# Kernel optimization log

Hardware: AMD Instinct MI355X
Metric: run time of the kernel (lower is better)

Reference implementation:

```python
import jax, jax.numpy as jnp
import numpy as np

B, S, E, HEADS = 2, 2048, 2048, 16


def setup_inputs() -> dict:
    key = jax.random.key(0)
    k1, k2, k3 = jax.random.split(key, 3)
    x = jax.random.normal(k1, (B, S, E), dtype=jnp.float32)
    # Linear weights stored as (in, out); torch uses y = x @ W.T with W (out, in) -- same math.
    W_qkvh = jax.random.normal(k2, (E, 3 * E + HEADS), dtype=jnp.float32) * (E ** -0.5)
    W_out = jax.random.normal(k3, (E, E), dtype=jnp.float32) * (E ** -0.5)
    return {"x": x, "W_qkvh": W_qkvh, "W_out": W_out}


def reference(x, W_qkvh, W_out):
    b, s, e = x.shape
    heads = W_qkvh.shape[1] - 3 * e
    d = e // heads
    scale = e ** 0.5

    proj = x @ W_qkvh                                  # (b, s, 3e + heads)
    QKV, Hg = proj[..., : 3 * e], proj[..., 3 * e:]
    Hg = jnp.tanh(Hg).transpose(0, 2, 1)[..., None]    # (b, h, s, 1) gate
    QKV = QKV.reshape(b, s, heads, 3 * d).transpose(0, 2, 1, 3)  # (b, h, s, 3d)
    Q, K, V = jnp.split(QKV, 3, axis=-1)               # each (b, h, s, d)

    # Cummean(H*K) along seq: cumsum(n * x) / n^2 with n = 1..s
    n = jnp.arange(1, s + 1, dtype=x.dtype).reshape(1, 1, s, 1)
    Kc = jnp.cumsum(n * (Hg * K), axis=2) / (n * n)    # (b, h, s, d)

    scores = jnp.einsum('bhqd,bhkd->bhqk', Q, Kc) / scale
    causal = jnp.triu(jnp.ones((s, s), dtype=bool), k=1)
    scores = jnp.where(causal, -jnp.inf, scores)
    attn = jax.nn.softmax(scores, axis=-1)

    out = jnp.einsum('bhqk,bhkd->bhqd', attn, V)       # (b, h, s, d)
    out = out.transpose(0, 2, 1, 3).reshape(b, s, e)
    return out @ W_out
```

## Files before the change

kernel.cpp:

```cpp
#include <hip/hip_runtime.h>
#include <hip/hip_bf16.h>
#include <math.h>

#define PB 2
#define PS 2048
#define PE 2048
#define PH 16
#define PD 128
#define PN_PROJ 6160
#define PM 4096

typedef __attribute__((ext_vector_type(8))) short bf16x8;
typedef __attribute__((ext_vector_type(4))) float f32x4;

__device__ __forceinline__ void gload_lds16(const void* g, void* l) {
  __builtin_amdgcn_global_load_lds((const __attribute__((address_space(1))) void*)g,
                                   (__attribute__((address_space(3))) void*)l, 16, 0, 0);
}

__global__ __launch_bounds__(512, 1) void gemm_qkv(
    const __hip_bfloat16* __restrict__ A, const __hip_bfloat16* __restrict__ Bt,
    __hip_bfloat16* __restrict__ Qp, __hip_bfloat16* __restrict__ Kp,
    __hip_bfloat16* __restrict__ Vtp, int K, int nTilesX) {
  constexpr int BM = 128, BN = 384, WM = 2, WN = 4;
  constexpr int MF = BM / WM / 16;
  constexpr int NF = BN / WN / 16;
  constexpr int SLOT = (BM + BN) * 64;
  constexpr int AL = BM / 64;
  constexpr int BL = BN / 64;
  constexpr int NLD = AL + BL;

  __shared__ __align__(16) __hip_bfloat16 lds[2 * SLOT];

  const int tid = threadIdx.x;
  const int w = tid >> 6, lane = tid & 63;
  const int fq = lane >> 4, fr = lane & 15;
  const int wm = w / WN, wn = w % WN;

  const int xcd = blockIdx.x & 7;
  const int local = blockIdx.x >> 3;
  const int h = xcd * 2 + (local >> 5);
  const int mBase = (local & 31) * BM;
  const int nBase = h * BN;

  const int srow = tid >> 3, sc = tid & 7;

  auto stage = [&](int t) {
    char* base = (char*)lds + (size_t)(t & 1) * SLOT * 2;
#pragma unroll
    for (int l = 0; l < AL; ++l) {
      int row = l * 64 + srow;
      int cs = sc ^ (row & 7);
      gload_lds16(A + (size_t)(mBase + row) * K + t * 64 + cs * 8,
                  base + l * 8192 + w * 1024);
    }
#pragma unroll
    for (int l = 0; l < BL; ++l) {
      int row = l * 64 + srow;
      int cs = sc ^ (row & 7);
      gload_lds16(Bt + (size_t)(nBase + row) * K + t * 64 + cs * 8,
                  base + BM * 128 + l * 8192 + w * 1024);
    }
  };

  f32x4 acc[MF][NF];
#pragma unroll
  for (int m = 0; m < MF; ++m)
#pragma unroll
    for (int n = 0; n < NF; ++n) acc[m][n] = (f32x4){0.f, 0.f, 0.f, 0.f};

  const int NT = K / 64;
  stage(0); stage(1);

#pragma unroll 1
  for (int t = 0; t < NT; ++t) {
    if (t + 1 < NT) asm volatile("s_waitcnt vmcnt(%0)" ::"i"(NLD) : "memory");
    else            asm volatile("s_waitcnt vmcnt(0)" ::: "memory");
    __builtin_amdgcn_s_barrier();
    __builtin_amdgcn_sched_barrier(0);

    const __hip_bfloat16* sl = lds + (size_t)(t & 1) * SLOT;

    bf16x8 av[MF], bv[NF];
#pragma unroll
    for (int m = 0; m < MF; ++m) {
      int row = wm * (BM / WM) + m * 16 + fr;
      av[m] = *(const bf16x8*)&sl[row * 64 + ((fq ^ (row & 7)) * 8)];
    }
#pragma unroll
    for (int n = 0; n < NF; ++n) {
      int row = wn * (BN / WN) + n * 16 + fr;
      bv[n] = *(const bf16x8*)&sl[BM * 64 + row * 64 + ((fq ^ (row & 7)) * 8)];
    }
    asm volatile("s_waitcnt lgkmcnt(0)" ::: "memory");
    __builtin_amdgcn_sched_barrier(0);
    __builtin_amdgcn_s_setprio(1);
#pragma unroll
    for (int m = 0; m < MF; ++m)
#pragma unroll
      for (int n = 0; n < NF; ++n)
        acc[m][n] = __builtin_amdgcn_mfma_f32_16x16x32_bf16(av[m], bv[n], acc[m][n], 0, 0, 0);
    __builtin_amdgcn_s_setprio(0);

#pragma unroll
    for (int m = 0; m < MF; ++m) {
      int row = wm * (BM / WM) + m * 16 + fr;
      av[m] = *(const bf16x8*)&sl[row * 64 + (((4 + fq) ^ (row & 7)) * 8)];
    }
#pragma unroll
    for (int n = 0; n < NF; ++n) {
      int row = wn * (BN / WN) + n * 16 + fr;
      bv[n] = *(const bf16x8*)&sl[BM * 64 + row * 64 + (((4 + fq) ^ (row & 7)) * 8)];
    }
    asm volatile("s_waitcnt lgkmcnt(0)" ::: "memory");
    __builtin_amdgcn_s_barrier();
    __builtin_amdgcn_sched_barrier(0);
    if (t + 2 < NT) stage(t + 2);
    __builtin_amdgcn_s_setprio(1);
#pragma unroll
    for (int m = 0; m < MF; ++m)
#pragma unroll
      for (int n = 0; n < NF; ++n)
        acc[m][n] = __builtin_amdgcn_mfma_f32_16x16x32_bf16(av[m], bv[n], acc[m][n], 0, 0, 0);
    __builtin_amdgcn_s_setprio(0);
  }

#pragma unroll
  for (int m = 0; m < MF; ++m) {
#pragma unroll
    for (int n = 0; n < NF; ++n) {
      int row0 = mBase + wm * (BM / WM) + m * 16 + fq * 4;
      int colL = wn * (BN / WN) + n * 16 + fr;
      int which = colL >> 7;
      int d = colL & 127;
      int b = row0 >> 11, s0 = row0 & (PS - 1);
      if (which == 2) {
        union { __hip_bfloat16 hh[4]; uint2 u; } pk;
#pragma unroll
        for (int j = 0; j < 4; ++j) pk.hh[j] = __float2bfloat16(acc[m][n][j]);
        *(uint2*)&Vtp[(((size_t)(b * PH + h)) * PD + d) * PS + s0] = pk.u;
      } else {
        __hip_bfloat16* dst = which == 0 ? Qp : Kp;
#pragma unroll
        for (int j = 0; j < 4; ++j)
          dst[(((size_t)(b * PH + h)) * PS + s0 + j) * PD + d] = __float2bfloat16(acc[m][n][j]);
      }
    }
  }
}

template <int BM, int BN, int WM, int WN, typename OutT>
__global__ __launch_bounds__(512, 1) void gemm_cs3(
    const __hip_bfloat16* __restrict__ A, const __hip_bfloat16* __restrict__ Bt,
    OutT* __restrict__ C, int K, int lda, int ldb, int ldc, int nTilesX) {
  constexpr int MF = BM / WM / 16;
  constexpr int NF = BN / WN / 16;
  constexpr int SLOT = (BM + BN) * 64;
  constexpr int AL = BM / 64;
  constexpr int BL = BN / 64;
  constexpr int NLD = AL + BL;

  __shared__ __align__(16) __hip_bfloat16 lds[3 * SLOT];

  const int tid = threadIdx.x;
  const int w = tid >> 6, lane = tid & 63;
  const int fq = lane >> 4, fr = lane & 15;
  const int wm = w / WN, wn = w % WN;

  const int xcd = blockIdx.x & 7;
  const int local = blockIdx.x >> 3;
  const int nPerX = nTilesX >> 3;
  const int nTY = (gridDim.x >> 3) / nPerX;
  const int mBase = (local % nTY) * BM;
  const int nBase = (xcd * nPerX + local / nTY) * BN;

  const int srow = tid >> 3, sc = tid & 7;

  auto stage = [&](int t) {
    char* base = (char*)lds + (size_t)(t % 3) * SLOT * 2;
#pragma unroll
    for (int l = 0; l < AL; ++l) {
      int row = l * 64 + srow;
      int cs = sc ^ (row & 7);
      gload_lds16(A + (size_t)(mBase + row) * lda + t * 64 + cs * 8,
                  base + l * 8192 + w * 1024);
    }
#pragma unroll
    for (int l = 0; l < BL; ++l) {
      int row = l * 64 + srow;
      int cs = sc ^ (row & 7);
      gload_lds16(Bt + (size_t)(nBase + row) * ldb + t * 64 + cs * 8,
                  base + BM * 128 + l * 8192 + w * 1024);
    }
  };

  f32x4 acc[MF][NF];
#pragma unroll
  for (int m = 0; m < MF; ++m)
#pragma unroll
    for (int n = 0; n < NF; ++n) acc[m][n] = (f32x4){0.f, 0.f, 0.f, 0.f};

  const int NT = K / 64;
  stage(0); stage(1);

#pragma unroll 1
  for (int t = 0; t < NT; ++t) {
    if (t + 1 < NT) asm volatile("s_waitcnt vmcnt(%0)" ::"i"(NLD) : "memory");
    else            asm volatile("s_waitcnt vmcnt(0)" ::: "memory");
    __builtin_amdgcn_s_barrier();
    __builtin_amdgcn_sched_barrier(0);
    if (t + 2 < NT) stage(t + 2);

    const __hip_bfloat16* sl = lds + (size_t)(t % 3) * SLOT;

#pragma unroll
    for (int kk = 0; kk < 2; ++kk) {
      bf16x8 av[MF], bv[NF];
#pragma unroll
      for (int m = 0; m < MF; ++m) {
        int row = wm * (BM / WM) + m * 16 + fr;
        av[m] = *(const bf16x8*)&sl[row * 64 + (((kk * 4 + fq) ^ (row & 7)) * 8)];
      }
#pragma unroll
      for (int n = 0; n < NF; ++n) {
        int row = wn * (BN / WN) + n * 16 + fr;
        bv[n] = *(const bf16x8*)&sl[BM * 64 + row * 64 + (((kk * 4 + fq) ^ (row & 7)) * 8)];
      }
      asm volatile("s_waitcnt lgkmcnt(0)" ::: "memory");
      __builtin_amdgcn_sched_barrier(0);
      __builtin_amdgcn_s_setprio(1);
#pragma unroll
      for (int m = 0; m < MF; ++m)
#pragma unroll
        for (int n = 0; n < NF; ++n)
          acc[m][n] = __builtin_amdgcn_mfma_f32_16x16x32_bf16(av[m], bv[n], acc[m][n], 0, 0, 0);
      __builtin_amdgcn_s_setprio(0);
    }
  }

#pragma unroll
  for (int m = 0; m < MF; ++m) {
#pragma unroll
    for (int n = 0; n < NF; ++n) {
      int row0 = mBase + wm * (BM / WM) + m * 16 + fq * 4;
      int col = nBase + wn * (BN / WN) + n * 16 + fr;
#pragma unroll
      for (int j = 0; j < 4; ++j) {
        if constexpr (__is_same(OutT, float))
          C[(size_t)(row0 + j) * ldc + col] = acc[m][n][j];
        else
          C[(size_t)(row0 + j) * ldc + col] = __float2bfloat16(acc[m][n][j]);
      }
    }
  }
}

__global__ __launch_bounds__(256) void transpose_cast(const float* __restrict__ W,
                                                      __hip_bfloat16* __restrict__ Wt,
                                                      int ldw, int ldt, int nOff) {
  __shared__ float t[32][33];
  int nb = blockIdx.x * 32, kb = blockIdx.y * 32;
  int tx = threadIdx.x & 31, ty = threadIdx.x >> 5;
#pragma unroll
  for (int i = 0; i < 4; ++i) {
    int k = ty + i * 8;
    t[k][tx] = W[(size_t)(kb + k) * ldw + nOff + nb + tx];
  }
  __syncthreads();
#pragma unroll
  for (int i = 0; i < 4; ++i) {
    int n = ty + i * 8;
    Wt[(size_t)(nb + n) * ldt + kb + tx] = __float2bfloat16(t[tx][n]);
  }
}

__global__ __launch_bounds__(256) void hg_from_x(const float* __restrict__ x,
                                                 const float* __restrict__ W,
                                                 float* __restrict__ hgbuf,
                                                 __hip_bfloat16* __restrict__ xb) {
  int bs = blockIdx.x;
  int b = bs >> 11, s = bs & (PS - 1);
  __shared__ float xs[PE];
  __shared__ float red[16][17];
  const float* xr = x + (size_t)bs * PE;
  for (int i = threadIdx.x; i < PE / 4; i += 256)
    *(float4*)&xs[i * 4] = ((const float4*)xr)[i];
  __syncthreads();
  {
    union { __hip_bfloat16 hh[8]; bf16x8 v; } pk;
#pragma unroll
    for (int k = 0; k < 8; ++k) pk.hh[k] = __float2bfloat16(xs[threadIdx.x * 8 + k]);
    *(bf16x8*)&xb[(size_t)bs * PE + threadIdx.x * 8] = pk.v;
  }
  int h = threadIdx.x & 15, part = threadIdx.x >> 4;
  float acc = 0.f;
  for (int k = part * 128; k < part * 128 + 128; ++k)
    acc += xs[k] * W[(size_t)k * PN_PROJ + 3 * PE + h];
  red[part][h] = acc;
  __syncthreads();
  if (threadIdx.x < 16) {
    float sm = 0.f;
#pragma unroll
    for (int p = 0; p < 16; ++p) sm += red[p][threadIdx.x];
    hgbuf[(size_t)(b * PH + threadIdx.x) * PS + s] = tanhf(sm);
  }
}

#define KC_SCALE 0.031879358f

__global__ __launch_bounds__(128) void kc_pass1(const __hip_bfloat16* __restrict__ Kp,
                                                const float* __restrict__ hgbuf,
                                                float* __restrict__ csum) {
  int c = blockIdx.x & 15, bh = blockIdx.x >> 4;
  int d = threadIdx.x;
  __shared__ float hgs[128];
  hgs[d] = hgbuf[(size_t)bh * PS + c * 128 + d];
  __syncthreads();
  const __hip_bfloat16* kb = Kp + ((size_t)bh * PS + c * 128) * PD + d;
  float acc = 0.f;
  int j0 = c * 128;
  for (int i = 0; i < 128; ++i)
    acc += (float)(j0 + i + 1) * hgs[i] * __bfloat162float(kb[(size_t)i * PD]);
  csum[blockIdx.x * 128 + d] = acc;
}

__global__ __launch_bounds__(128) void kc_pass2(__hip_bfloat16* __restrict__ Kp,
                                                const float* __restrict__ hgbuf,
                                                const float* __restrict__ csum) {
  int c = blockIdx.x & 15, bh = blockIdx.x >> 4;
  int d = threadIdx.x;
  __shared__ float hgs[128];
  hgs[d] = hgbuf[(size_t)bh * PS + c * 128 + d];
  __syncthreads();
  float acc = 0.f;
  for (int cc = 0; cc < c; ++cc) acc += csum[(bh * 16 + cc) * 128 + d];
  __hip_bfloat16* kb = Kp + ((size_t)bh * PS + c * 128) * PD + d;
  int j0 = c * 128;
  for (int i = 0; i < 128; ++i) {
    float t = (float)(j0 + i + 1);
    acc += t * hgs[i] * __bfloat162float(kb[(size_t)i * PD]);
    kb[(size_t)i * PD] = __float2bfloat16(acc / (t * t) * KC_SCALE);
  }
}

__global__ __launch_bounds__(512, 1) void attn_mfma(const __hip_bfloat16* __restrict__ Qp,
                                                    const __hip_bfloat16* __restrict__ Kp,
                                                    const __hip_bfloat16* __restrict__ Vtp,
                                                    __hip_bfloat16* __restrict__ O) {
  const int qt = 15 - (blockIdx.x >> 5);
  const int bh = blockIdx.x & 31;
  const int b = bh >> 4, h = bh & 15;
  const int tid = threadIdx.x;
  const int w = tid >> 6, lane = tid & 63;
  const int fq = lane >> 4, fr = lane & 15;
  const int nt = (qt + 1) * 2;
  const int q0 = qt * 128;
  const int qw = q0 + w * 16;

  __shared__ __align__(16) char smem[67584];
  __hip_bfloat16* Psw = (__hip_bfloat16*)(smem + 49152) + w * 16 * 72;
  __hip_bfloat16* Os = (__hip_bfloat16*)(smem + 16384);

  const __hip_bfloat16* kb0 = Kp + (size_t)bh * PS * PD;
  const __hip_bfloat16* vb0 = Vtp + (size_t)bh * PD * PS;

  auto stageK = [&](int t, int bufi) {
    char* ksb = smem + bufi * 16384;
    const __hip_bfloat16* kb = kb0 + (size_t)(t * 64) * PD;
#pragma unroll
    for (int p = 0; p < 2; ++p) {
      int s = p * 512 + tid;
      int row = s >> 4, c = s & 15;
      int cs = c ^ (row & 7);
      gload_lds16(kb + (size_t)row * PD + cs * 8,
                  ksb + (size_t)(p * 512 + (tid & ~63)) * 16);
    }
  };
  auto stageV = [&](int t) {
    char* vsb = smem + 32768;
    const __hip_bfloat16* vb = vb0 + t * 64;
#pragma unroll
    for (int p = 0; p < 2; ++p) {
      int s = p * 512 + tid;
      int row = s >> 3, c = s & 7;
      int cs = c ^ (row & 7);
      gload_lds16(vb + (size_t)row * PS + cs * 8,
                  vsb + (size_t)(p * 512 + (tid & ~63)) * 16);
    }
  };

  const __hip_bfloat16* qbase = Qp + ((size_t)bh * PS + qw) * PD;
  bf16x8 qf[4];
#pragma unroll
  for (int kk = 0; kk < 4; ++kk)
    qf[kk] = *(const bf16x8*)&qbase[(size_t)fr * PD + kk * 32 + fq * 8];

  stageK(0, 0);
  stageV(0);
  int cur = 0;

  f32x4 oacc[8];
#pragma unroll
  for (int nd = 0; nd < 8; ++nd) oacc[nd] = (f32x4){0.f, 0.f, 0.f, 0.f};
  float m_ = -__builtin_inff(), l_ = 0.f;

#pragma unroll 1
  for (int kt = 0; kt < nt; ++kt) {
    const bool hasNextK = (kt + 1 < nt);
    if (hasNextK) stageK(kt + 1, cur ^ 1);
    if (hasNextK) asm volatile("s_waitcnt vmcnt(4)" ::: "memory");
    else          asm volatile("s_waitcnt vmcnt(2)" ::: "memory");
    __builtin_amdgcn_s_barrier();
    __builtin_amdgcn_sched_barrier(0);

    const bool compute = (kt * 64 <= qw + 15);
    const bool diag = (kt * 64 + 63) > qw;
    const __hip_bfloat16* Ks = (const __hip_bfloat16*)(smem + cur * 16384);

    f32x4 sacc[4];
    if (compute) {
#pragma unroll
      for (int n = 0; n < 4; ++n) sacc[n] = (f32x4){0.f, 0.f, 0.f, 0.f};
#pragma unroll
      for (int kk = 0; kk < 4; ++kk) {
#pragma unroll
        for (int n = 0; n < 4; ++n) {
          bf16x8 kf = *(const bf16x8*)&Ks[(n * 16 + fr) * 128 + (((kk * 4 + fq) ^ (fr & 7)) * 8)];
          sacc[n] = __builtin_amdgcn_mfma_f32_16x16x32_bf16(kf, qf[kk], sacc[n], 0, 0, 0);
        }
      }
    }

    if (hasNextK) asm volatile("s_waitcnt vmcnt(2)" ::: "memory");
    else          asm volatile("s_waitcnt vmcnt(0)" ::: "memory");
    __builtin_amdgcn_s_barrier();
    __builtin_amdgcn_sched_barrier(0);

    if (compute) {
      const __hip_bfloat16* Vts = (const __hip_bfloat16*)(smem + 32768);
      const int qg = qw + fr;
      float sv[4][4];
#pragma unroll
      for (int n = 0; n < 4; ++n)
#pragma unroll
        for (int j = 0; j < 4; ++j) sv[n][j] = sacc[n][j];
      if (diag) {
#pragma unroll
        for (int n = 0; n < 4; ++n)
#pragma unroll
          for (int j = 0; j < 4; ++j)
            if ((kt * 64 + n * 16 + fq * 4 + j) > qg) sv[n][j] = -__builtin_inff();
      }
      float pmax = sv[0][0];
#pragma unroll
      for (int n = 0; n < 4; ++n)
#pragma unroll
        for (int j = 0; j < 4; ++j) pmax = fmaxf(pmax, sv[n][j]);
      pmax = fmaxf(pmax, __shfl_xor(pmax, 16, 64));
      pmax = fmaxf(pmax, __shfl_xor(pmax, 32, 64));

      const bool nof = __all(pmax <= m_ + 11.5415605f);
      const float mn = nof ? m_ : fmaxf(m_, pmax);
      float ps = 0.f;
#pragma unroll
      for (int n = 0; n < 4; ++n) {
        union { __hip_bfloat16 hh[4]; uint2 u; } pkk;
#pragma unroll
        for (int j = 0; j < 4; ++j) {
          float p = exp2f(sv[n][j] - mn);
          ps += p;
          pkk.hh[j] = __float2bfloat16(p);
        }
        *(uint2*)&Psw[fr * 72 + n * 16 + fq * 4] = pkk.u;
      }
      ps += __shfl_xor(ps, 16, 64);
      ps += __shfl_xor(ps, 32, 64);

      if (!nof) {
        const float alpha = exp2f(m_ - mn);
        l_ = l_ * alpha + ps;
        m_ = mn;
        float a0 = __shfl(alpha, fq * 4 + 0, 64);
        float a1 = __shfl(alpha, fq * 4 + 1, 64);
        float a2 = __shfl(alpha, fq * 4 + 2, 64);
        float a3 = __shfl(alpha, fq * 4 + 3, 64);
#pragma unroll
        for (int nd = 0; nd < 8; ++nd) {
          oacc[nd][0] *= a0; oacc[nd][1] *= a1;
          oacc[nd][2] *= a2; oacc[nd][3] *= a3;
        }
      } else {
        l_ += ps;
      }

#pragma unroll
      for (int kk2 = 0; kk2 < 2; ++kk2) {
        bf16x8 pa = *(const bf16x8*)&Psw[fr * 72 + kk2 * 32 + fq * 8];
#pragma unroll
        for (int nd = 0; nd < 8; ++nd) {
          bf16x8 vf = *(const bf16x8*)&Vts[(nd * 16 + fr) * 64 + (((kk2 * 4 + fq) ^ (fr & 7)) * 8)];
          oacc[nd] = __builtin_amdgcn_mfma_f32_16x16x32_bf16(pa, vf, oacc[nd], 0, 0, 0);
        }
      }
    }

    asm volatile("s_waitcnt lgkmcnt(0)" ::: "memory");
    __builtin_amdgcn_sched_barrier(0);
    __builtin_amdgcn_s_barrier();
    if (kt + 1 < nt) stageV(kt + 1);
    cur ^= 1;
  }

  float inv = 1.0f / l_;
  float inv4[4];
#pragma unroll
  for (int j = 0; j < 4; ++j) inv4[j] = __shfl(inv, fq * 4 + j, 64);
#pragma unroll
  for (int nd = 0; nd < 8; ++nd)
#pragma unroll
    for (int j = 0; j < 4; ++j)
      Os[(w * 16 + fq * 4 + j) * 136 + nd * 16 + fr] =
          __float2bfloat16(oacc[nd][j] * inv4[j]);
  __syncthreads();
#pragma unroll
  for (int it = 0; it < 4; ++it) {
    int i = it * 512 + tid;
    int row = i >> 4, ch = i & 15;
    *(bf16x8*)&O[(size_t)(b * PS + q0 + row) * PE + h * 128 + ch * 8] =
        *(const bf16x8*)&Os[row * 136 + ch * 8];
  }
}

extern "C" void kernel_launch(void* const* d_in, const int* in_sizes, int n_in,
                              void* d_out, int out_size, void* d_ws, size_t ws_size,
                              hipStream_t stream) {
  const float* x     = (const float*)d_in[0];
  const float* Wqkvh = (const float*)d_in[1];
  const float* Wout  = (const float*)d_in[2];
  float* out = (float*)d_out;

  const size_t HD = (size_t)PB * PH * PS * PD;
  char* wsb = (char*)d_ws;
  __hip_bfloat16* Qp = (__hip_bfloat16*)wsb;   wsb += HD * 2;
  __hip_bfloat16* Kp = (__hip_bfloat16*)wsb;   wsb += HD * 2;
  __hip_bfloat16* Vtp = (__hip_bfloat16*)wsb;  wsb += HD * 2;
  __hip_bfloat16* xb = (__hip_bfloat16*)wsb;   wsb += (size_t)PM * PE * 2;
  __hip_bfloat16* Wq_t = (__hip_bfloat16*)wsb; wsb += (size_t)3 * PE * PE * 2;
  __hip_bfloat16* Wout_t = (__hip_bfloat16*)wsb; wsb += (size_t)PE * PE * 2;
  float* hgbuf = (float*)wsb;                  wsb += (size_t)PB * PH * PS * 4;
  float* csum = (float*)wsb;

  hg_from_x<<<PM, 256, 0, stream>>>(x, Wqkvh, hgbuf, xb);
  transpose_cast<<<dim3(3 * PE / 32, PE / 32), 256, 0, stream>>>(Wqkvh, Wq_t, PN_PROJ, PE, 0);
  transpose_cast<<<dim3(PE / 32, PE / 32), 256, 0, stream>>>(Wout, Wout_t, PE, PE, 0);

  gemm_qkv<<<dim3((PM / 128) * PH), 512, 0, stream>>>(xb, Wq_t, Qp, Kp, Vtp, PE, PH);

  kc_pass1<<<PB * PH * 16, 128, 0, stream>>>(Kp, hgbuf, csum);
  kc_pass2<<<PB * PH * 16, 128, 0, stream>>>(Kp, hgbuf, csum);

  __hip_bfloat16* Ob = xb;
  attn_mfma<<<512, 512, 0, stream>>>(Qp, Kp, Vtp, Ob);

  gemm_cs3<128, 256, 2, 4, float>
      <<<dim3((PM / 128) * (PE / 256)), 512, 0, stream>>>(
          Ob, Wout_t, out, PE, PE, PE, PE, PE / 256);
}
```

Before: 294.7 us.

## Pair complementary causal query tiles per attention block for load balance

Each attention block now processes two query tiles, pk and 15-pk, sharing the K/V tiles staged into LDS across the longer tile's key range, and the grid is halved to 256 blocks. This evens out per-block work under the causal mask and reuses each staged K/V tile for two query groups. In exchange it doubles the accumulator and Q-fragment registers per thread, which risks spills under 512-thread launch bounds, and leaves fewer blocks to spread over the CUs.

```diff
diff --git a/kernel.cpp b/kernel.cpp
--- a/kernel.cpp
+++ b/kernel.cpp
@@ -347,15 +347,17 @@
                                                     const __hip_bfloat16* __restrict__ Kp,
                                                     const __hip_bfloat16* __restrict__ Vtp,
                                                     __hip_bfloat16* __restrict__ O) {
-  const int qt = 15 - (blockIdx.x >> 5);
+  const int pk = blockIdx.x >> 5;
   const int bh = blockIdx.x & 31;
   const int b = bh >> 4, h = bh & 15;
   const int tid = threadIdx.x;
   const int w = tid >> 6, lane = tid & 63;
   const int fq = lane >> 4, fr = lane & 15;
-  const int nt = (qt + 1) * 2;
-  const int q0 = qt * 128;
-  const int qw = q0 + w * 16;
+  const int qtg[2] = {pk, 15 - pk};
+  const int nt = (qtg[1] + 1) * 2;
+  int qw2[2];
+#pragma unroll
+  for (int g = 0; g < 2; ++g) qw2[g] = qtg[g] * 128 + w * 16;
 
   __shared__ __align__(16) char smem[67584];
   __hip_bfloat16* Psw = (__hip_bfloat16*)(smem + 49152) + w * 16 * 72;
@@ -389,20 +391,26 @@
     }
   };
 
-  const __hip_bfloat16* qbase = Qp + ((size_t)bh * PS + qw) * PD;
-  bf16x8 qf[4];
-#pragma unroll
-  for (int kk = 0; kk < 4; ++kk)
-    qf[kk] = *(const bf16x8*)&qbase[(size_t)fr * PD + kk * 32 + fq * 8];
+  bf16x8 qf[2][4];
+#pragma unroll
+  for (int g = 0; g < 2; ++g) {
+    const __hip_bfloat16* qbase = Qp + ((size_t)bh * PS + qw2[g]) * PD;
+#pragma unroll
+    for (int kk = 0; kk < 4; ++kk)
+      qf[g][kk] = *(const bf16x8*)&qbase[(size_t)fr * PD + kk * 32 + fq * 8];
+  }
 
   stageK(0, 0);
   stageV(0);
   int cur = 0;
 
-  f32x4 oacc[8];
-#pragma unroll
-  for (int nd = 0; nd < 8; ++nd) oacc[nd] = (f32x4){0.f, 0.f, 0.f, 0.f};
-  float m_ = -__builtin_inff(), l_ = 0.f;
+  f32x4 oacc[2][8];
+#pragma unroll
+  for (int g = 0; g < 2; ++g)
+#pragma unroll
+    for (int nd = 0; nd < 8; ++nd) oacc[g][nd] = (f32x4){0.f, 0.f, 0.f, 0.f};
+  float m_[2] = {-__builtin_inff(), -__builtin_inff()};
+  float l_[2] = {0.f, 0.f};
 
 #pragma unroll 1
   for (int kt = 0; kt < nt; ++kt) {
@@ -413,20 +421,24 @@
     __builtin_amdgcn_s_barrier();
     __builtin_amdgcn_sched_barrier(0);
 
-    const bool compute = (kt * 64 <= qw + 15);
-    const bool diag = (kt * 64 + 63) > qw;
     const __hip_bfloat16* Ks = (const __hip_bfloat16*)(smem + cur * 16384);
-
-    f32x4 sacc[4];
-    if (compute) {
-#pragma unroll
-      for (int n = 0; n < 4; ++n) sacc[n] = (f32x4){0.f, 0.f, 0.f, 0.f};
-#pragma unroll
-      for (int kk = 0; kk < 4; ++kk) {
-#pragma unroll
-        for (int n = 0; n < 4; ++n) {
-          bf16x8 kf = *(const bf16x8*)&Ks[(n * 16 + fr) * 128 + (((kk * 4 + fq) ^ (fr & 7)) * 8)];
-          sacc[n] = __builtin_amdgcn_mfma_f32_16x16x32_bf16(kf, qf[kk], sacc[n], 0, 0, 0);
+    bool computeg[2];
+#pragma unroll
+    for (int g = 0; g < 2; ++g) computeg[g] = (kt * 64 <= qw2[g] + 15);
+
+    f32x4 sacc[2][4];
+#pragma unroll
+    for (int g = 0; g < 2; ++g) {
+      if (computeg[g]) {
+#pragma unroll
+        for (int n = 0; n < 4; ++n) sacc[g][n] = (f32x4){0.f, 0.f, 0.f, 0.f};
+#pragma unroll
+        for (int kk = 0; kk < 4; ++kk) {
+#pragma unroll
+          for (int n = 0; n < 4; ++n) {
+            bf16x8 kf = *(const bf16x8*)&Ks[(n * 16 + fr) * 128 + (((kk * 4 + fq) ^ (fr & 7)) * 8)];
+            sacc[g][n] = __builtin_amdgcn_mfma_f32_16x16x32_bf16(kf, qf[g][kk], sacc[g][n], 0, 0, 0);
+          }
         }
       }
     }
@@ -436,70 +448,74 @@
     __builtin_amdgcn_s_barrier();
     __builtin_amdgcn_sched_barrier(0);
 
-    if (compute) {
-      const __hip_bfloat16* Vts = (const __hip_bfloat16*)(smem + 32768);
-      const int qg = qw + fr;
-      float sv[4][4];
-#pragma unroll
-      for (int n = 0; n < 4; ++n)
-#pragma unroll
-        for (int j = 0; j < 4; ++j) sv[n][j] = sacc[n][j];
-      if (diag) {
+    const __hip_bfloat16* Vts = (const __hip_bfloat16*)(smem + 32768);
+#pragma unroll
+    for (int g = 0; g < 2; ++g) {
+      if (computeg[g]) {
+        const bool diag = (kt * 64 + 63) > qw2[g];
+        const int qg = qw2[g] + fr;
+        float sv[4][4];
 #pragma unroll
         for (int n = 0; n < 4; ++n)
 #pragma unroll
-          for (int j = 0; j < 4; ++j)
-            if ((kt * 64 + n * 16 + fq * 4 + j) > qg) sv[n][j] = -__builtin_inff();
-      }
-      float pmax = sv[0][0];
-#pragma unroll
-      for (int n = 0; n < 4; ++n)
-#pragma unroll
-        for (int j = 0; j < 4; ++j) pmax = fmaxf(pmax, sv[n][j]);
-      pmax = fmaxf(pmax, __shfl_xor(pmax, 16, 64));
-      pmax = fmaxf(pmax, __shfl_xor(pmax, 32, 64));
-
-      const bool nof = __all(pmax <= m_ + 11.5415605f);
-      const float mn = nof ? m_ : fmaxf(m_, pmax);
-      float ps = 0.f;
-#pragma unroll
-      for (int n = 0; n < 4; ++n) {
-        union { __hip_bfloat16 hh[4]; uint2 u; } pkk;
-#pragma unroll
-        for (int j = 0; j < 4; ++j) {
-          float p = exp2f(sv[n][j] - mn);
-          ps += p;
-          pkk.hh[j] = __float2bfloat16(p);
+          for (int j = 0; j < 4; ++j) sv[n][j] = sacc[g][n][j];
+        if (diag) {
+#pragma unroll
+          for (int n = 0; n < 4; ++n)
+#pragma unroll
+            for (int j = 0; j < 4; ++j)
+              if ((kt * 64 + n * 16 + fq * 4 + j) > qg) sv[n][j] = -__builtin_inff();
         }
-        *(uint2*)&Psw[fr * 72 + n * 16 + fq * 4] = pkk.u;
-      }
-      ps += __shfl_xor(ps, 16, 64);
-      ps += __shfl_xor(ps, 32, 64);
-
-      if (!nof) {
-        const float alpha = exp2f(m_ - mn);
-        l_ = l_ * alpha + ps;
-        m_ = mn;
-        float a0 = __shfl(alpha, fq * 4 + 0, 64);
-        float a1 = __shfl(alpha, fq * 4 + 1, 64);
-        float a2 = __shfl(alpha, fq * 4 + 2, 64);
-        float a3 = __shfl(alpha, fq * 4 + 3, 64);
-#pragma unroll
-        for (int nd = 0; nd < 8; ++nd) {
-          oacc[nd][0] *= a0; oacc[nd][1] *= a1;
-          oacc[nd][2] *= a2; oacc[nd][3] *= a3;
+        float pmax = sv[0][0];
+#pragma unroll
+        for (int n = 0; n < 4; ++n)
+#pragma unroll
+          for (int j = 0; j < 4; ++j) pmax = fmaxf(pmax, sv[n][j]);
+        pmax = fmaxf(pmax, __shfl_xor(pmax, 16, 64));
+        pmax = fmaxf(pmax, __shfl_xor(pmax, 32, 64));
+
+        const bool nof = __all(pmax <= m_[g] + 11.5415605f);
+        const float mn = nof ? m_[g] : fmaxf(m_[g], pmax);
+        float ps = 0.f;
+#pragma unroll
+        for (int n = 0; n < 4; ++n) {
+          union { __hip_bfloat16 hh[4]; uint2 u; } pkk;
+#pragma unroll
+          for (int j = 0; j < 4; ++j) {
+            float p = exp2f(sv[n][j] - mn);
+            ps += p;
+            pkk.hh[j] = __float2bfloat16(p);
+          }
+          *(uint2*)&Psw[fr * 72 + n * 16 + fq * 4] = pkk.u;
         }
-      } else {
-        l_ += ps;
-      }
-
-#pragma unroll
-      for (int kk2 = 0; kk2 < 2; ++kk2) {
-        bf16x8 pa = *(const bf16x8*)&Psw[fr * 72 + kk2 * 32 + fq * 8];
-#pragma unroll
-        for (int nd = 0; nd < 8; ++nd) {
-          bf16x8 vf = *(const bf16x8*)&Vts[(nd * 16 + fr) * 64 + (((kk2 * 4 + fq) ^ (fr & 7)) * 8)];
-          oacc[nd] = __builtin_amdgcn_mfma_f32_16x16x32_bf16(pa, vf, oacc[nd], 0, 0, 0);
+        ps += __shfl_xor(ps, 16, 64);
+        ps += __shfl_xor(ps, 32, 64);
+
+        if (!nof) {
+          const float alpha = exp2f(m_[g] - mn);
+          l_[g] = l_[g] * alpha + ps;
+          m_[g] = mn;
+          float a0 = __shfl(alpha, fq * 4 + 0, 64);
+          float a1 = __shfl(alpha, fq * 4 + 1, 64);
+          float a2 = __shfl(alpha, fq * 4 + 2, 64);
+          float a3 = __shfl(alpha, fq * 4 + 3, 64);
+#pragma unroll
+          for (int nd = 0; nd < 8; ++nd) {
+            oacc[g][nd][0] *= a0; oacc[g][nd][1] *= a1;
+            oacc[g][nd][2] *= a2; oacc[g][nd][3] *= a3;
+          }
+        } else {
+          l_[g] += ps;
+        }
+
+#pragma unroll
+        for (int kk2 = 0; kk2 < 2; ++kk2) {
+          bf16x8 pa = *(const bf16x8*)&Psw[fr * 72 + kk2 * 32 + fq * 8];
+#pragma unroll
+          for (int nd = 0; nd < 8; ++nd) {
+            bf16x8 vf = *(const bf16x8*)&Vts[(nd * 16 + fr) * 64 + (((kk2 * 4 + fq) ^ (fr & 7)) * 8)];
+            oacc[g][nd] = __builtin_amdgcn_mfma_f32_16x16x32_bf16(pa, vf, oacc[g][nd], 0, 0, 0);
+          }
         }
       }
     }
@@ -511,23 +527,27 @@
     cur ^= 1;
   }
 
-  float inv = 1.0f / l_;
-  float inv4[4];
-#pragma unroll
-  for (int j = 0; j < 4; ++j) inv4[j] = __shfl(inv, fq * 4 + j, 64);
-#pragma unroll
-  for (int nd = 0; nd < 8; ++nd)
-#pragma unroll
-    for (int j = 0; j < 4; ++j)
-      Os[(w * 16 + fq * 4 + j) * 136 + nd * 16 + fr] =
-          __float2bfloat16(oacc[nd][j] * inv4[j]);
-  __syncthreads();
-#pragma unroll
-  for (int it = 0; it < 4; ++it) {
-    int i = it * 512 + tid;
-    int row = i >> 4, ch = i & 15;
-    *(bf16x8*)&O[(size_t)(b * PS + q0 + row) * PE + h * 128 + ch * 8] =
-        *(const bf16x8*)&Os[row * 136 + ch * 8];
+#pragma unroll 1
+  for (int g = 0; g < 2; ++g) {
+    float inv = 1.0f / l_[g];
+    float inv4[4];
+#pragma unroll
+    for (int j = 0; j < 4; ++j) inv4[j] = __shfl(inv, fq * 4 + j, 64);
+#pragma unroll
+    for (int nd = 0; nd < 8; ++nd)
+#pragma unroll
+      for (int j = 0; j < 4; ++j)
+        Os[(w * 16 + fq * 4 + j) * 136 + nd * 16 + fr] =
+            __float2bfloat16(oacc[g][nd][j] * inv4[j]);
+    __syncthreads();
+#pragma unroll
+    for (int it = 0; it < 4; ++it) {
+      int i = it * 512 + tid;
+      int row = i >> 4, ch = i & 15;
+      *(bf16x8*)&O[(size_t)(b * PS + qtg[g] * 128 + row) * PE + h * 128 + ch * 8] =
+          *(const bf16x8*)&Os[row * 136 + ch * 8];
+    }
+    __syncthreads();
   }
 }
 
@@ -560,7 +580,7 @@
   kc_pass2<<<PB * PH * 16, 128, 0, stream>>>(Kp, hgbuf, csum);
 
   __hip_bfloat16* Ob = xb;
-  attn_mfma<<<512, 512, 0, stream>>>(Qp, Kp, Vtp, Ob);
+  attn_mfma<<<256, 512, 0, stream>>>(Qp, Kp, Vtp, Ob);
 
   gemm_cs3<128, 256, 2, 4, float>
       <<<dim3((PM / 128) * (PE / 256)), 512, 0, stream>>>(
```

Result: slower. 308.4 us (+4.7%).
